# Kernel tuning notes

Measured on AMD Instinct MI355X. Metric: run time of the kernel, lower is better.

The kernel has to match this reference:

```python
import jax, jax.numpy as jnp
import numpy as np

LAYER_SIZE = 8
STACK_SIZE = 2
RES_CH = 64
SKIP_CH = 128
N = 16
L = 8192
NUM_BLOCKS = LAYER_SIZE * STACK_SIZE


def _dilations():
    return [2 ** lev for _ in range(STACK_SIZE) for lev in range(LAYER_SIZE)]


def setup_inputs() -> dict:
    key = jax.random.key(0)
    k1, k2, k3, k4 = jax.random.split(key, 4)
    x = jax.random.normal(k1, (N, RES_CH, L), dtype=jnp.float32)
    # conv weights scaled ~1/sqrt(fan_in) to keep gates in a sane range
    W_dil = jax.random.normal(k2, (NUM_BLOCKS, RES_CH, RES_CH, 2), dtype=jnp.float32) * 0.088
    W_res = jax.random.normal(k3, (NUM_BLOCKS, RES_CH, RES_CH), dtype=jnp.float32) * 0.125
    W_skip = jax.random.normal(k4, (NUM_BLOCKS, SKIP_CH, RES_CH), dtype=jnp.float32) * 0.125
    return {"x": x, "W_dil": W_dil, "W_res": W_res, "W_skip": W_skip}


def reference(x, W_dil, W_res, W_skip):
    dilations = _dilations()
    out = x
    skips = []
    for i, d in enumerate(dilations):
        wd = W_dil[i]    # (Cout, Cin, 2)
        wr = W_res[i]    # (C, C) 1x1
        ws = W_skip[i]   # (S, C) 1x1
        # dilated causal conv, kernel_size=2, no padding -> length L-d
        y = (jnp.einsum('oi,nil->nol', wd[:, :, 0], out[:, :, :-d])
             + jnp.einsum('oi,nil->nol', wd[:, :, 1], out[:, :, d:]))
        # gated activation: tanh and sigmoid of the SAME dilated output
        g = jnp.tanh(y) * jax.nn.sigmoid(y)
        # NOTE: source has `if self.pooling > 1` with self.pooling a bool,
        # so AvgPool1d is never applied; pool_out == g always.
        res = jnp.einsum('oi,nil->nol', wr, g) + out[:, :, -g.shape[2]:]
        skips.append(jnp.einsum('oi,nil->nol', ws, g))
        out = res
    osize = out.shape[2]
    skip_out = skips[0][:, :, -osize:]
    for s in skips[1:]:
        skip_out = skip_out + s[:, :, -osize:]
    return (out, skip_out)
```

## Files before the change

### kernel.cpp

```cpp
#include <hip/hip_runtime.h>


#define NBATCH 16
#define C 64
#define SC 128
#define L0 8192
#define OSIZE 7682
#define TILE 64
#define ST 128

typedef __bf16 bf16x8 __attribute__((ext_vector_type(8)));
typedef __bf16 bf16x4 __attribute__((ext_vector_type(4)));
typedef float  f32x4  __attribute__((ext_vector_type(4)));

__global__ __launch_bounds__(256) void pack_weights(
    const float* __restrict__ Wd, const float* __restrict__ Wr,
    const float* __restrict__ Ws,
    __bf16* __restrict__ Wdm, __bf16* __restrict__ Wrm, __bf16* __restrict__ Wsm)
{
    int idx = blockIdx.x * 256 + threadIdx.x;
    if (idx < 131072) {
        int kp = idx & 127, o = (idx >> 7) & 63, ly = idx >> 13;
        int k = kp & 63, tap = kp >> 6;
        Wdm[idx] = (__bf16)Wd[(((ly * 64 + o) * 64 + k) << 1) + tap];
    } else if (idx < 196608) {
        int j = idx - 131072;
        Wrm[j] = (__bf16)Wr[j];
    } else if (idx < 327680) {
        int j = idx - 196608;
        Wsm[j] = (__bf16)Ws[j];
    }
}

__global__ __launch_bounds__(256) void wavenet_layer_mfma(
    const float* __restrict__ src, int src_stride, int Lin,
    float* __restrict__ dst, int dst_stride,
    const __bf16* __restrict__ Wdm,
    const __bf16* __restrict__ Wrm,
    __bf16* __restrict__ gout,
    int d)
{
    extern __shared__ char smem_raw[];
    const int W    = TILE + d;
    const int Lout = Lin - d;
    const int n  = blockIdx.y;
    const int l0 = blockIdx.x * TILE;
    if (l0 >= Lout) return;
    const int np = min(TILE, Lout - l0);

    __bf16* sxp  = (__bf16*)smem_raw;
    float*  sres = (float*)(smem_raw + (size_t)8 * W * 8 * 2);
    __bf16* sgp  = (__bf16*)(sres + 64 * 65);

    const int t    = threadIdx.x;
    const int lane = t & 63;
    const int wv   = t >> 6;
    const int q    = lane >> 4;
    const int nn   = lane & 15;

    for (int item = t; item < 8 * W; item += 256) {
        int kg = item / W;
        int p  = item % W;
        bool inb = (l0 + p) < Lin;
        const float* col = src + (size_t)(n * C + kg * 8) * src_stride + l0 + p;
        float v[8];
        #pragma unroll
        for (int j = 0; j < 8; ++j) v[j] = inb ? col[(size_t)j * src_stride] : 0.f;
        bf16x8 bv;
        #pragma unroll
        for (int j = 0; j < 8; ++j) bv[j] = (__bf16)v[j];
        *(bf16x8*)(sxp + ((size_t)kg * W + p) * 8) = bv;
        int pr = p - d;
        if (pr >= 0 && pr < TILE) {
            #pragma unroll
            for (int j = 0; j < 8; ++j) sres[(kg * 8 + j) * 65 + pr] = v[j];
        }
    }
    __syncthreads();

    const __bf16* arow = Wdm + (size_t)(wv * 16 + nn) * 128 + q * 8;
    bf16x8 aW[4];
    #pragma unroll
    for (int ks = 0; ks < 4; ++ks) aW[ks] = *(const bf16x8*)(arow + ks * 32);

    #pragma unroll
    for (int nt = 0; nt < 4; ++nt) {
        int p0 = nt * 16;
        f32x4 acc = {0.f, 0.f, 0.f, 0.f};
        acc = __builtin_amdgcn_mfma_f32_16x16x32_bf16(aW[0],
                *(const bf16x8*)(sxp + ((size_t)(q    ) * W + p0 + nn    ) * 8), acc, 0, 0, 0);
        acc = __builtin_amdgcn_mfma_f32_16x16x32_bf16(aW[1],
                *(const bf16x8*)(sxp + ((size_t)(4 + q) * W + p0 + nn    ) * 8), acc, 0, 0, 0);
        acc = __builtin_amdgcn_mfma_f32_16x16x32_bf16(aW[2],
                *(const bf16x8*)(sxp + ((size_t)(q    ) * W + p0 + nn + d) * 8), acc, 0, 0, 0);
        acc = __builtin_amdgcn_mfma_f32_16x16x32_bf16(aW[3],
                *(const bf16x8*)(sxp + ((size_t)(4 + q) * W + p0 + nn + d) * 8), acc, 0, 0, 0);
        bf16x4 gv;
        #pragma unroll
        for (int r = 0; r < 4; ++r) {
            float y = fminf(fmaxf(acc[r], -20.f), 20.f);
            float u = __expf(y);
            gv[r] = (__bf16)(u * (u - 1.f) / fmaf(u, u, 1.f));
        }
        *(bf16x4*)(sgp + ((size_t)(2 * wv + (q >> 1)) * 64 + p0 + nn) * 8 + (q & 1) * 4) = gv;
    }
    __syncthreads();

    const __bf16* rrow = Wrm + (size_t)(wv * 16 + nn) * 64 + q * 8;
    bf16x8 aR0 = *(const bf16x8*)rrow;
    bf16x8 aR1 = *(const bf16x8*)(rrow + 32);
    #pragma unroll
    for (int nt = 0; nt < 4; ++nt) {
        int p0 = nt * 16;
        f32x4 acc = {0.f, 0.f, 0.f, 0.f};
        acc = __builtin_amdgcn_mfma_f32_16x16x32_bf16(aR0,
                *(const bf16x8*)(sgp + ((size_t)(q    ) * 64 + p0 + nn) * 8), acc, 0, 0, 0);
        acc = __builtin_amdgcn_mfma_f32_16x16x32_bf16(aR1,
                *(const bf16x8*)(sgp + ((size_t)(4 + q) * 64 + p0 + nn) * 8), acc, 0, 0, 0);
        if (p0 + nn < np) {
            #pragma unroll
            for (int r = 0; r < 4; ++r) {
                int ch = wv * 16 + q * 4 + r;
                dst[(size_t)(n * C + ch) * dst_stride + l0 + p0 + nn]
                    = acc[r] + sres[ch * 65 + p0 + nn];
            }
        }
    }

    const int sbase = Lout - OSIZE;
    for (int item = t; item < 8 * TILE; item += 256) {
        int p  = item & 63;
        int kg = item >> 6;
        int l  = l0 + p;
        if (l >= sbase && l < Lout) {
            *(bf16x8*)(gout + (((size_t)n * 8 + kg) * OSIZE + (l - sbase)) * 8)
                = *(const bf16x8*)(sgp + ((size_t)kg * 64 + p) * 8);
        }
    }
}

__global__ __launch_bounds__(256) void skip_gemm(
    const __bf16* __restrict__ g,
    const __bf16* __restrict__ Wsm,
    float* __restrict__ skip,
    int G, int lybase, int init)
{
    __shared__ __bf16 Bb[8][ST][8];
    const int n  = blockIdx.y;
    const int l0 = blockIdx.x * ST;
    const int t  = threadIdx.x;
    const int lane = t & 63;
    const int wv   = __builtin_amdgcn_readfirstlane(t >> 6);
    const int q = lane >> 4, nn = lane & 15;

    f32x4 acc[2][8];
    #pragma unroll
    for (int mt = 0; mt < 2; ++mt)
        #pragma unroll
        for (int nt = 0; nt < 8; ++nt) acc[mt][nt] = (f32x4){0.f, 0.f, 0.f, 0.f};

    for (int gi = 0; gi < G; ++gi) {
        const __bf16* gl = g + ((size_t)gi * NBATCH + n) * (size_t)8 * OSIZE * 8;
        #pragma unroll
        for (int j = 0; j < 4; ++j) {
            int kg   = 2 * wv + (j >> 1);
            int half = j & 1;
            const __bf16* srcp = gl + ((size_t)kg * OSIZE + l0 + half * 64) * 8
                                    + (size_t)lane * 8;
            __builtin_amdgcn_global_load_lds(
                (const __attribute__((address_space(1))) void*)srcp,
                (__attribute__((address_space(3))) void*)&Bb[kg][half * 64][0],
                16, 0, 0);
        }
        const __bf16* Wl = Wsm + (size_t)(lybase + gi) * SC * 64;
        bf16x8 a00 = *(const bf16x8*)(Wl + (size_t)(wv * 32 +      nn) * 64 +  0 + q * 8);
        bf16x8 a01 = *(const bf16x8*)(Wl + (size_t)(wv * 32 +      nn) * 64 + 32 + q * 8);
        bf16x8 a10 = *(const bf16x8*)(Wl + (size_t)(wv * 32 + 16 + nn) * 64 +  0 + q * 8);
        bf16x8 a11 = *(const bf16x8*)(Wl + (size_t)(wv * 32 + 16 + nn) * 64 + 32 + q * 8);
        __syncthreads();
        #pragma unroll
        for (int ks = 0; ks < 2; ++ks) {
            #pragma unroll
            for (int nt = 0; nt < 8; ++nt) {
                bf16x8 b = *(const bf16x8*)&Bb[ks * 4 + q][nt * 16 + nn][0];
                acc[0][nt] = __builtin_amdgcn_mfma_f32_16x16x32_bf16(
                                 ks ? a01 : a00, b, acc[0][nt], 0, 0, 0);
                acc[1][nt] = __builtin_amdgcn_mfma_f32_16x16x32_bf16(
                                 ks ? a11 : a10, b, acc[1][nt], 0, 0, 0);
            }
        }
        __syncthreads();
    }

    #pragma unroll
    for (int mt = 0; mt < 2; ++mt)
        #pragma unroll
        for (int nt = 0; nt < 8; ++nt) {
            int p = l0 + nt * 16 + nn;
            if (p < OSIZE) {
                #pragma unroll
                for (int r = 0; r < 4; ++r) {
                    int s = wv * 32 + mt * 16 + q * 4 + r;
                    size_t idx = ((size_t)n * SC + s) * OSIZE + p;
                    float v = acc[mt][nt][r];
                    skip[idx] = init ? v : (skip[idx] + v);
                }
            }
        }
}

extern "C" void kernel_launch(void* const* d_in, const int* in_sizes, int n_in,
                              void* d_out, int out_size, void* d_ws, size_t ws_size,
                              hipStream_t stream) {
    const float* x      = (const float*)d_in[0];
    const float* W_dil  = (const float*)d_in[1];
    const float* W_res  = (const float*)d_in[2];
    const float* W_skip = (const float*)d_in[3];

    float* out  = (float*)d_out;
    float* skip = out + (size_t)NBATCH * C * OSIZE;

    float*  bufA = (float*)d_ws;
    float*  bufB = bufA + (size_t)NBATCH * C * L0;
    __bf16* Wdm  = (__bf16*)(bufB + (size_t)NBATCH * C * L0);
    __bf16* Wrm  = Wdm + 16 * 64 * 128;
    __bf16* Wsm  = Wrm + 16 * 64 * 64;
    __bf16* gst  = Wsm + 16 * 128 * 64;

    const size_t slotHW = (size_t)NBATCH * 8 * OSIZE * 8;
    const size_t used   = (size_t)((char*)gst - (char*)d_ws);
    int G = 16;
    while (G > 1 && used + (size_t)G * slotHW * 2 + 65536 > ws_size) G >>= 1;

    pack_weights<<<1280, 256, 0, stream>>>(W_dil, W_res, W_skip, Wdm, Wrm, Wsm);

    const float* src = x;
    int src_stride = L0, Lin = L0;
    float* bufs[2] = {bufA, bufB};

    for (int i = 0; i < 16; ++i) {
        int d    = 1 << (i & 7);
        int Lout = Lin - d;
        float* dst;
        int dst_stride;
        if (i == 15) { dst = out;         dst_stride = OSIZE; }
        else         { dst = bufs[i & 1]; dst_stride = L0;    }

        int W = TILE + d;
        size_t smem = (size_t)128 * W + 64 * 65 * 4 + 8 * 64 * 8 * 2;

        dim3 grid((Lout + TILE - 1) / TILE, NBATCH);
        wavenet_layer_mfma<<<grid, 256, smem, stream>>>(
            src, src_stride, Lin, dst, dst_stride,
            Wdm + (size_t)i * 64 * 128,
            Wrm + (size_t)i * 64 * 64,
            gst + (size_t)(i % G) * slotHW,
            d);

        if (((i + 1) % G) == 0) {
            dim3 sgrid((OSIZE + ST - 1) / ST, NBATCH);
            skip_gemm<<<sgrid, 256, 0, stream>>>(
                gst, Wsm, skip, G, i + 1 - G, (i + 1 == G) ? 1 : 0);
        }

        src = dst;
        src_stride = dst_stride;
        Lin = Lout;
    }
}
```

Measured before the change: 602.3 us.

## Fuse all sixteen layers into one cooperative kernel with register-resident skip accumulation

Replaces the per-layer kernel launches with a single cooperative kernel. Each block owns a fixed 256-sample tile of one batch row, runs all 16 layers with grid-wide syncs between them, and keeps the skip-sum accumulators in registers so the gated activations are never written to or reread from global memory. This removes per-layer launch overhead and the global traffic for skip contributions. In exchange it needs all 512 blocks co-resident (2 per CU), carries a large register footprint for the skip accumulators, and pays a grid barrier per layer. The path computes every position in the tile (clamped at the left edge) and trims the causal prefix only at the output.

```diff
diff --git a/kernel.cpp b/kernel.cpp
--- a/kernel.cpp
+++ b/kernel.cpp
@@ -1,4 +1,7 @@
 #include <hip/hip_runtime.h>
+#include <hip/hip_cooperative_groups.h>
+
+namespace cg = cooperative_groups;
 
 
 #define NBATCH 16
@@ -8,6 +11,9 @@
 #define OSIZE 7682
 #define TILE 64
 #define ST 128
+#define FT 256
+#define FW 384
+#define FSMEM (8*FW*8*2 + 8*FT*8*2)
 
 typedef __bf16 bf16x8 __attribute__((ext_vector_type(8)));
 typedef __bf16 bf16x4 __attribute__((ext_vector_type(4)));
@@ -32,6 +38,149 @@
     }
 }
 
+__global__ __launch_bounds__(256, 2) void wavenet_fused(
+    const float* __restrict__ x,
+    float* __restrict__ bufA, float* __restrict__ bufB,
+    const __bf16* __restrict__ Wdm, const __bf16* __restrict__ Wrm,
+    const __bf16* __restrict__ Wsm,
+    float* __restrict__ out, float* __restrict__ skip)
+{
+    extern __shared__ char smem[];
+    __bf16* sxp = (__bf16*)smem;
+    __bf16* sgp = (__bf16*)(smem + 8 * FW * 8 * 2);
+
+    cg::grid_group gg = cg::this_grid();
+
+    const int blk = blockIdx.x;
+    const int n   = blk >> 5;
+    const int a   = (blk & 31) * FT;
+    const int t    = threadIdx.x;
+    const int lane = t & 63;
+    const int wv   = t >> 6;
+    const int q    = lane >> 4;
+    const int nn   = lane & 15;
+
+    f32x4 accS[2][16];
+    #pragma unroll
+    for (int mt = 0; mt < 2; ++mt)
+        #pragma unroll
+        for (int nt = 0; nt < 16; ++nt)
+            accS[mt][nt] = (f32x4){0.f, 0.f, 0.f, 0.f};
+
+    const float* src = x;
+
+    for (int ly = 0; ly < 16; ++ly) {
+        const int d = 1 << (ly & 7);
+        const int W = FT + d;
+
+        for (int kg = 0; kg < 8; ++kg) {
+            for (int j = t; j < W; j += 256) {
+                int s = a - d + j;
+                if (s < 0) s = 0;
+                const float* col = src + (size_t)(n * C + kg * 8) * L0 + s;
+                bf16x8 bv;
+                #pragma unroll
+                for (int jj = 0; jj < 8; ++jj) bv[jj] = (__bf16)col[(size_t)jj * L0];
+                *(bf16x8*)(sxp + ((size_t)kg * FW + j) * 8) = bv;
+            }
+        }
+        __syncthreads();
+
+        const __bf16* arow = Wdm + ((size_t)ly * 64 + (wv * 16 + nn)) * 128 + q * 8;
+        bf16x8 aW0 = *(const bf16x8*)(arow);
+        bf16x8 aW1 = *(const bf16x8*)(arow + 32);
+        bf16x8 aW2 = *(const bf16x8*)(arow + 64);
+        bf16x8 aW3 = *(const bf16x8*)(arow + 96);
+        #pragma unroll 4
+        for (int nt = 0; nt < 16; ++nt) {
+            int p = nt * 16 + nn;
+            f32x4 acc = {0.f, 0.f, 0.f, 0.f};
+            acc = __builtin_amdgcn_mfma_f32_16x16x32_bf16(aW0,
+                    *(const bf16x8*)(sxp + ((size_t)(q    ) * FW + p    ) * 8), acc, 0, 0, 0);
+            acc = __builtin_amdgcn_mfma_f32_16x16x32_bf16(aW1,
+                    *(const bf16x8*)(sxp + ((size_t)(4 + q) * FW + p    ) * 8), acc, 0, 0, 0);
+            acc = __builtin_amdgcn_mfma_f32_16x16x32_bf16(aW2,
+                    *(const bf16x8*)(sxp + ((size_t)(q    ) * FW + p + d) * 8), acc, 0, 0, 0);
+            acc = __builtin_amdgcn_mfma_f32_16x16x32_bf16(aW3,
+                    *(const bf16x8*)(sxp + ((size_t)(4 + q) * FW + p + d) * 8), acc, 0, 0, 0);
+            bf16x4 gv;
+            #pragma unroll
+            for (int r = 0; r < 4; ++r) {
+                float y = fminf(fmaxf(acc[r], -20.f), 20.f);
+                float u = __expf(y);
+                gv[r] = (__bf16)(u * (u - 1.f) / fmaf(u, u, 1.f));
+            }
+            *(bf16x4*)(sgp + ((size_t)(2 * wv + (q >> 1)) * FT + p) * 8 + (q & 1) * 4) = gv;
+        }
+        __syncthreads();
+
+        const __bf16* rrow = Wrm + ((size_t)ly * 64 + (wv * 16 + nn)) * 64 + q * 8;
+        bf16x8 aR0 = *(const bf16x8*)rrow;
+        bf16x8 aR1 = *(const bf16x8*)(rrow + 32);
+        float* dst = (ly & 1) ? bufB : bufA;
+        #pragma unroll 4
+        for (int nt = 0; nt < 16; ++nt) {
+            int p = nt * 16 + nn;
+            f32x4 acc = {0.f, 0.f, 0.f, 0.f};
+            acc = __builtin_amdgcn_mfma_f32_16x16x32_bf16(aR0,
+                    *(const bf16x8*)(sgp + ((size_t)(q    ) * FT + p) * 8), acc, 0, 0, 0);
+            acc = __builtin_amdgcn_mfma_f32_16x16x32_bf16(aR1,
+                    *(const bf16x8*)(sgp + ((size_t)(4 + q) * FT + p) * 8), acc, 0, 0, 0);
+            int s = a + p;
+            if (ly == 15) {
+                if (s >= 510) {
+                    #pragma unroll
+                    for (int r = 0; r < 4; ++r) {
+                        int ch = wv * 16 + q * 4 + r;
+                        out[(size_t)(n * C + ch) * OSIZE + (s - 510)]
+                            = acc[r] + src[(size_t)(n * C + ch) * L0 + s];
+                    }
+                }
+            } else {
+                #pragma unroll
+                for (int r = 0; r < 4; ++r) {
+                    int ch = wv * 16 + q * 4 + r;
+                    dst[(size_t)(n * C + ch) * L0 + s]
+                        = acc[r] + src[(size_t)(n * C + ch) * L0 + s];
+                }
+            }
+        }
+
+        const __bf16* srow = Wsm + (size_t)ly * SC * 64;
+        bf16x8 aS00 = *(const bf16x8*)(srow + (size_t)(wv * 32 +      nn) * 64 +      q * 8);
+        bf16x8 aS01 = *(const bf16x8*)(srow + (size_t)(wv * 32 +      nn) * 64 + 32 + q * 8);
+        bf16x8 aS10 = *(const bf16x8*)(srow + (size_t)(wv * 32 + 16 + nn) * 64 +      q * 8);
+        bf16x8 aS11 = *(const bf16x8*)(srow + (size_t)(wv * 32 + 16 + nn) * 64 + 32 + q * 8);
+        #pragma unroll
+        for (int nt = 0; nt < 16; ++nt) {
+            int p = nt * 16 + nn;
+            bf16x8 b0 = *(const bf16x8*)(sgp + ((size_t)(q    ) * FT + p) * 8);
+            bf16x8 b1 = *(const bf16x8*)(sgp + ((size_t)(4 + q) * FT + p) * 8);
+            accS[0][nt] = __builtin_amdgcn_mfma_f32_16x16x32_bf16(aS00, b0, accS[0][nt], 0, 0, 0);
+            accS[0][nt] = __builtin_amdgcn_mfma_f32_16x16x32_bf16(aS01, b1, accS[0][nt], 0, 0, 0);
+            accS[1][nt] = __builtin_amdgcn_mfma_f32_16x16x32_bf16(aS10, b0, accS[1][nt], 0, 0, 0);
+            accS[1][nt] = __builtin_amdgcn_mfma_f32_16x16x32_bf16(aS11, b1, accS[1][nt], 0, 0, 0);
+        }
+
+        src = dst;
+        if (ly < 15) gg.sync();
+    }
+
+    #pragma unroll
+    for (int mt = 0; mt < 2; ++mt)
+        #pragma unroll
+        for (int nt = 0; nt < 16; ++nt) {
+            int s = a + nt * 16 + nn;
+            if (s >= 510) {
+                #pragma unroll
+                for (int r = 0; r < 4; ++r) {
+                    int sch = wv * 32 + mt * 16 + q * 4 + r;
+                    skip[(size_t)(n * SC + sch) * OSIZE + (s - 510)] = accS[mt][nt][r];
+                }
+            }
+        }
+}
+
 __global__ __launch_bounds__(256) void wavenet_layer_mfma(
     const float* __restrict__ src, int src_stride, int Lin,
     float* __restrict__ dst, int dst_stride,
@@ -227,12 +376,32 @@
     __bf16* Wsm  = Wrm + 16 * 64 * 64;
     __bf16* gst  = Wsm + 16 * 128 * 64;
 
+    static int use_coop = -1;
+    if (use_coop < 0) {
+        int dev = 0, coop = 0, nb = 0;
+        hipGetDevice(&dev);
+        hipDeviceGetAttribute(&coop, hipDeviceAttributeCooperativeLaunch, dev);
+        hipError_t e = hipOccupancyMaxActiveBlocksPerMultiprocessor(
+            &nb, (const void*)wavenet_fused, 256, FSMEM);
+        use_coop = (coop && e == hipSuccess && nb >= 2) ? 1 : 0;
+    }
+
+    pack_weights<<<1280, 256, 0, stream>>>(W_dil, W_res, W_skip, Wdm, Wrm, Wsm);
+
+    if (use_coop) {
+        void* args[] = { (void*)&x, (void*)&bufA, (void*)&bufB,
+                         (void*)&Wdm, (void*)&Wrm, (void*)&Wsm,
+                         (void*)&out, (void*)&skip };
+        hipLaunchCooperativeKernel((const void*)wavenet_fused,
+                                   dim3(NBATCH * (L0 / FT)), dim3(256),
+                                   args, FSMEM, stream);
+        return;
+    }
+
     const size_t slotHW = (size_t)NBATCH * 8 * OSIZE * 8;
     const size_t used   = (size_t)((char*)gst - (char*)d_ws);
     int G = 16;
     while (G > 1 && used + (size_t)G * slotHW * 2 + 65536 > ws_size) G >>= 1;
-
-    pack_weights<<<1280, 256, 0, stream>>>(W_dil, W_res, W_skip, Wdm, Wrm, Wsm);
 
     const float* src = x;
     int src_stride = L0, Lin = L0;
```

Result: no change. 601.3 us (-0.2%).

## Drop residual LDS staging and double-buffer skip GEMM loads

Applied to the files above, without the earlier changes.

The layer kernel no longer copies the fp32 residual into shared memory. It re-reads the residual from global memory (likely an L2 hit) when writing the output, which cuts the LDS footprint by about 16KB so more blocks can reside per CU. The skip GEMM now double-buffers its global-to-LDS loads so the next layer's g tile is fetched while MFMAs run on the current one. Both kernels also gain a launch-bounds min-blocks hint of 4. The risks are extra global traffic for the residual reads and higher register pressure from the occupancy hint.

```diff
diff --git a/kernel.cpp b/kernel.cpp
--- a/kernel.cpp
+++ b/kernel.cpp
@@ -32,7 +32,7 @@
     }
 }
 
-__global__ __launch_bounds__(256) void wavenet_layer_mfma(
+__global__ __launch_bounds__(256, 4) void wavenet_layer_mfma(
     const float* __restrict__ src, int src_stride, int Lin,
     float* __restrict__ dst, int dst_stride,
     const __bf16* __restrict__ Wdm,
@@ -48,9 +48,8 @@
     if (l0 >= Lout) return;
     const int np = min(TILE, Lout - l0);
 
-    __bf16* sxp  = (__bf16*)smem_raw;
-    float*  sres = (float*)(smem_raw + (size_t)8 * W * 8 * 2);
-    __bf16* sgp  = (__bf16*)(sres + 64 * 65);
+    __bf16* sxp = (__bf16*)smem_raw;
+    __bf16* sgp = sxp + (size_t)8 * W * 8;
 
     const int t    = threadIdx.x;
     const int lane = t & 63;
@@ -63,18 +62,10 @@
         int p  = item % W;
         bool inb = (l0 + p) < Lin;
         const float* col = src + (size_t)(n * C + kg * 8) * src_stride + l0 + p;
-        float v[8];
-        #pragma unroll
-        for (int j = 0; j < 8; ++j) v[j] = inb ? col[(size_t)j * src_stride] : 0.f;
         bf16x8 bv;
         #pragma unroll
-        for (int j = 0; j < 8; ++j) bv[j] = (__bf16)v[j];
+        for (int j = 0; j < 8; ++j) bv[j] = (__bf16)(inb ? col[(size_t)j * src_stride] : 0.f);
         *(bf16x8*)(sxp + ((size_t)kg * W + p) * 8) = bv;
-        int pr = p - d;
-        if (pr >= 0 && pr < TILE) {
-            #pragma unroll
-            for (int j = 0; j < 8; ++j) sres[(kg * 8 + j) * 65 + pr] = v[j];
-        }
     }
     __syncthreads();
 
@@ -118,11 +109,13 @@
         acc = __builtin_amdgcn_mfma_f32_16x16x32_bf16(aR1,
                 *(const bf16x8*)(sgp + ((size_t)(4 + q) * 64 + p0 + nn) * 8), acc, 0, 0, 0);
         if (p0 + nn < np) {
+            const float* sc = src + (size_t)(n * C + wv * 16 + q * 4) * src_stride
+                                  + l0 + d + p0 + nn;
             #pragma unroll
             for (int r = 0; r < 4; ++r) {
                 int ch = wv * 16 + q * 4 + r;
                 dst[(size_t)(n * C + ch) * dst_stride + l0 + p0 + nn]
-                    = acc[r] + sres[ch * 65 + p0 + nn];
+                    = acc[r] + sc[(size_t)r * src_stride];
             }
         }
     }
@@ -139,13 +132,13 @@
     }
 }
 
-__global__ __launch_bounds__(256) void skip_gemm(
+__global__ __launch_bounds__(256, 4) void skip_gemm(
     const __bf16* __restrict__ g,
     const __bf16* __restrict__ Wsm,
     float* __restrict__ skip,
     int G, int lybase, int init)
 {
-    __shared__ __bf16 Bb[8][ST][8];
+    __shared__ __bf16 Bb[2][8][ST][8];
     const int n  = blockIdx.y;
     const int l0 = blockIdx.x * ST;
     const int t  = threadIdx.x;
@@ -159,7 +152,7 @@
         #pragma unroll
         for (int nt = 0; nt < 8; ++nt) acc[mt][nt] = (f32x4){0.f, 0.f, 0.f, 0.f};
 
-    for (int gi = 0; gi < G; ++gi) {
+    auto stage = [&](int buf, int gi) {
         const __bf16* gl = g + ((size_t)gi * NBATCH + n) * (size_t)8 * OSIZE * 8;
         #pragma unroll
         for (int j = 0; j < 4; ++j) {
@@ -169,20 +162,27 @@
                                     + (size_t)lane * 8;
             __builtin_amdgcn_global_load_lds(
                 (const __attribute__((address_space(1))) void*)srcp,
-                (__attribute__((address_space(3))) void*)&Bb[kg][half * 64][0],
+                (__attribute__((address_space(3))) void*)&Bb[buf][kg][half * 64][0],
                 16, 0, 0);
         }
+    };
+
+    stage(0, 0);
+    __syncthreads();
+
+    for (int gi = 0; gi < G; ++gi) {
+        const int cur = gi & 1;
+        if (gi + 1 < G) stage(cur ^ 1, gi + 1);
         const __bf16* Wl = Wsm + (size_t)(lybase + gi) * SC * 64;
         bf16x8 a00 = *(const bf16x8*)(Wl + (size_t)(wv * 32 +      nn) * 64 +  0 + q * 8);
         bf16x8 a01 = *(const bf16x8*)(Wl + (size_t)(wv * 32 +      nn) * 64 + 32 + q * 8);
         bf16x8 a10 = *(const bf16x8*)(Wl + (size_t)(wv * 32 + 16 + nn) * 64 +  0 + q * 8);
         bf16x8 a11 = *(const bf16x8*)(Wl + (size_t)(wv * 32 + 16 + nn) * 64 + 32 + q * 8);
-        __syncthreads();
         #pragma unroll
         for (int ks = 0; ks < 2; ++ks) {
             #pragma unroll
             for (int nt = 0; nt < 8; ++nt) {
-                bf16x8 b = *(const bf16x8*)&Bb[ks * 4 + q][nt * 16 + nn][0];
+                bf16x8 b = *(const bf16x8*)&Bb[cur][ks * 4 + q][nt * 16 + nn][0];
                 acc[0][nt] = __builtin_amdgcn_mfma_f32_16x16x32_bf16(
                                  ks ? a01 : a00, b, acc[0][nt], 0, 0, 0);
                 acc[1][nt] = __builtin_amdgcn_mfma_f32_16x16x32_bf16(
@@ -247,7 +247,7 @@
         else         { dst = bufs[i & 1]; dst_stride = L0;    }
 
         int W = TILE + d;
-        size_t smem = (size_t)128 * W + 64 * 65 * 4 + 8 * 64 * 8 * 2;
+        size_t smem = (size_t)128 * W + 8 * 64 * 8 * 2;
 
         dim3 grid((Lout + TILE - 1) / TILE, NBATCH);
         wavenet_layer_mfma<<<grid, 256, smem, stream>>>(
```

Result: slower. 764.3 us (+26.9%).
